# Optimization experiments

Hardware: AMD Instinct MI355X
Metric: run time of the kernel (lower is better)

The kernel has to match this reference:

```python
import jax, jax.numpy as jnp
import numpy as np

N = 2_000_000
C0 = 0.28209479177387814
C1 = 0.4886025119029199


def setup_inputs() -> dict:
    key = jax.random.key(0)
    ks = jax.random.split(key, 6)
    return {
        "view_dirs": jax.random.normal(ks[0], (N, 3), dtype=jnp.float32),
        "xyz": jax.random.uniform(ks[1], (N, 3), dtype=jnp.float32) * 2.0 - 1.0,
        "scale_log": jax.random.uniform(ks[2], (N, 3), dtype=jnp.float32) - 3.0,
        "rot_quat": jax.random.uniform(ks[3], (N, 4), dtype=jnp.float32),
        "opacity_logit": jax.random.uniform(ks[4], (N, 1), dtype=jnp.float32),
        "sh_coeffs": jax.random.uniform(ks[5], (N, 3, 4), dtype=jnp.float32),
    }


def _build_rotation(q):
    # F.normalize along dim=1 with eps=1e-12
    q = q / jnp.maximum(jnp.linalg.norm(q, axis=1, keepdims=True), 1e-12)
    r, x, y, z = q[:, 0], q[:, 1], q[:, 2], q[:, 3]
    R = jnp.stack([
        1 - 2 * (y * y + z * z), 2 * (x * y - r * z), 2 * (x * z + r * y),
        2 * (x * y + r * z), 1 - 2 * (x * x + z * z), 2 * (y * z - r * x),
        2 * (x * z - r * y), 2 * (y * z + r * x), 1 - 2 * (x * x + y * y),
    ], axis=-1).reshape(-1, 3, 3)
    return R


def _eval_sh(sh_coeffs, dirs):
    # degree = 1 -> 4 coeffs
    x, y, z = dirs[:, 0:1], dirs[:, 1:2], dirs[:, 2:3]  # [N,1] broadcast over color
    return (C0 * sh_coeffs[:, :, 0]
            - C1 * y * sh_coeffs[:, :, 1]
            + C1 * z * sh_coeffs[:, :, 2]
            - C1 * x * sh_coeffs[:, :, 3])


def reference(view_dirs, xyz, scale_log, rot_quat, opacity_logit, sh_coeffs):
    opacity = jax.nn.sigmoid(opacity_logit)                  # [N,1]
    scale = jnp.exp(scale_log)                               # [N,3]
    rgb = jax.nn.sigmoid(_eval_sh(sh_coeffs, view_dirs))     # [N,3]
    R = _build_rotation(rot_quat)                            # [N,3,3]
    M = R * scale[:, None, :]                                # R @ diag(scale), columns scaled
    cov3d = jnp.einsum('nij,nkj->nik', M, M)                 # M @ M^T
    return xyz, cov3d, rgb, opacity
```

## Files before the change

### kernel.cpp

```cpp
#include <hip/hip_runtime.h>

#define C0 0.28209479177387814f
#define C1 0.4886025119029199f

__device__ __forceinline__ float sigmoidf(float x) {
    return 1.0f / (1.0f + expf(-x));
}

__global__ __launch_bounds__(256) void gauss_kernel(
    const float* __restrict__ view_dirs,
    const float* __restrict__ xyz,
    const float* __restrict__ scale_log,
    const float4* __restrict__ rot_quat,
    const float* __restrict__ opacity_logit,
    const float4* __restrict__ sh,
    float* __restrict__ out_xyz,
    float* __restrict__ out_cov,
    float* __restrict__ out_rgb,
    float* __restrict__ out_op,
    int N)
{
    int i = blockIdx.x * blockDim.x + threadIdx.x;
    if (i >= N) return;

    float vx = view_dirs[3*i+0], vy = view_dirs[3*i+1], vz = view_dirs[3*i+2];
    float px = xyz[3*i+0],       py = xyz[3*i+1],       pz = xyz[3*i+2];
    float sl0 = scale_log[3*i+0], sl1 = scale_log[3*i+1], sl2 = scale_log[3*i+2];
    float4 q  = rot_quat[i];
    float  ol = opacity_logit[i];
    float4 c0 = sh[3*i+0];
    float4 c1 = sh[3*i+1];
    float4 c2 = sh[3*i+2];

    float opacity = sigmoidf(ol);

    float r0 = C0*c0.x - C1*vy*c0.y + C1*vz*c0.z - C1*vx*c0.w;
    float r1 = C0*c1.x - C1*vy*c1.y + C1*vz*c1.z - C1*vx*c1.w;
    float r2 = C0*c2.x - C1*vy*c2.y + C1*vz*c2.z - C1*vx*c2.w;
    r0 = sigmoidf(r0); r1 = sigmoidf(r1); r2 = sigmoidf(r2);

    float nrm = sqrtf(q.x*q.x + q.y*q.y + q.z*q.z + q.w*q.w);
    float inv = 1.0f / fmaxf(nrm, 1e-12f);
    float r = q.x*inv, x = q.y*inv, y = q.z*inv, z = q.w*inv;

    float R00 = 1.0f - 2.0f*(y*y + z*z);
    float R01 = 2.0f*(x*y - r*z);
    float R02 = 2.0f*(x*z + r*y);
    float R10 = 2.0f*(x*y + r*z);
    float R11 = 1.0f - 2.0f*(x*x + z*z);
    float R12 = 2.0f*(y*z - r*x);
    float R20 = 2.0f*(x*z - r*y);
    float R21 = 2.0f*(y*z + r*x);
    float R22 = 1.0f - 2.0f*(x*x + y*y);

    float s0 = expf(sl0), s1 = expf(sl1), s2 = expf(sl2);

    float M00 = R00*s0, M01 = R01*s1, M02 = R02*s2;
    float M10 = R10*s0, M11 = R11*s1, M12 = R12*s2;
    float M20 = R20*s0, M21 = R21*s1, M22 = R22*s2;

    float cv00 = M00*M00 + M01*M01 + M02*M02;
    float cv01 = M00*M10 + M01*M11 + M02*M12;
    float cv02 = M00*M20 + M01*M21 + M02*M22;
    float cv11 = M10*M10 + M11*M11 + M12*M12;
    float cv12 = M10*M20 + M11*M21 + M12*M22;
    float cv22 = M20*M20 + M21*M21 + M22*M22;

    out_xyz[3*i+0] = px; out_xyz[3*i+1] = py; out_xyz[3*i+2] = pz;

    float* cp = out_cov + 9*i;
    cp[0] = cv00; cp[1] = cv01; cp[2] = cv02;
    cp[3] = cv01; cp[4] = cv11; cp[5] = cv12;
    cp[6] = cv02; cp[7] = cv12; cp[8] = cv22;

    out_rgb[3*i+0] = r0; out_rgb[3*i+1] = r1; out_rgb[3*i+2] = r2;
    out_op[i] = opacity;
}

extern "C" void kernel_launch(void* const* d_in, const int* in_sizes, int n_in,
                              void* d_out, int out_size, void* d_ws, size_t ws_size,
                              hipStream_t stream) {
    const float*  view_dirs     = (const float*)d_in[0];
    const float*  xyz           = (const float*)d_in[1];
    const float*  scale_log     = (const float*)d_in[2];
    const float4* rot_quat      = (const float4*)d_in[3];
    const float*  opacity_logit = (const float*)d_in[4];
    const float4* sh            = (const float4*)d_in[5];

    int N = in_sizes[4];

    float* out = (float*)d_out;
    float* out_xyz = out;
    float* out_cov = out + (size_t)3*N;
    float* out_rgb = out + (size_t)12*N;
    float* out_op  = out + (size_t)15*N;

    int block = 256;
    int grid = (N + block - 1) / block;
    gauss_kernel<<<grid, block, 0, stream>>>(view_dirs, xyz, scale_log, rot_quat,
                                             opacity_logit, sh,
                                             out_xyz, out_cov, out_rgb, out_op, N);
}
```

Before: 279.2 us.

## Stage strided AoS loads and stores through LDS for coalesced global access

Each block cooperatively loads view_dirs, scale_log and SH coefficients into shared memory with unit-stride coalesced reads, padding the SH layout to avoid bank conflicts. Results are staged back in LDS, and xyz, rgb and covariance are written with coalesced unit-stride stores. The aim is to remove the stride-3, stride-9 and stride-12 uncoalesced accesses in this memory-bound kernel. In exchange it adds three block barriers and about 20KB of LDS per block, which may lower occupancy.

```diff
diff --git a/kernel.cpp b/kernel.cpp
--- a/kernel.cpp
+++ b/kernel.cpp
@@ -2,79 +2,130 @@
 
 #define C0 0.28209479177387814f
 #define C1 0.4886025119029199f
+#define BLK 256
 
 __device__ __forceinline__ float sigmoidf(float x) {
     return 1.0f / (1.0f + expf(-x));
 }
 
-__global__ __launch_bounds__(256) void gauss_kernel(
+__global__ __launch_bounds__(BLK) void gauss_kernel_lds(
     const float* __restrict__ view_dirs,
     const float* __restrict__ xyz,
     const float* __restrict__ scale_log,
     const float4* __restrict__ rot_quat,
     const float* __restrict__ opacity_logit,
-    const float4* __restrict__ sh,
+    const float* __restrict__ sh,
     float* __restrict__ out_xyz,
     float* __restrict__ out_cov,
     float* __restrict__ out_rgb,
     float* __restrict__ out_op,
     int N)
 {
-    int i = blockIdx.x * blockDim.x + threadIdx.x;
-    if (i >= N) return;
+    __shared__ float lds_sh[BLK * 13];
+    __shared__ float lds_vd[BLK * 3];
+    __shared__ float lds_sl[BLK * 3];
 
-    float vx = view_dirs[3*i+0], vy = view_dirs[3*i+1], vz = view_dirs[3*i+2];
-    float px = xyz[3*i+0],       py = xyz[3*i+1],       pz = xyz[3*i+2];
-    float sl0 = scale_log[3*i+0], sl1 = scale_log[3*i+1], sl2 = scale_log[3*i+2];
-    float4 q  = rot_quat[i];
-    float  ol = opacity_logit[i];
-    float4 c0 = sh[3*i+0];
-    float4 c1 = sh[3*i+1];
-    float4 c2 = sh[3*i+2];
+    const int t    = threadIdx.x;
+    const int base = blockIdx.x * BLK;
+    const int nblk = min(BLK, N - base);
+    const long b3  = (long)base * 3;
+    const long b9  = (long)base * 9;
+    const long b12 = (long)base * 12;
 
-    float opacity = sigmoidf(ol);
+    #pragma unroll
+    for (int j = 0; j < 3; ++j) {
+        int f = t + BLK * j;
+        if (f < nblk * 3) {
+            lds_vd[f] = view_dirs[b3 + f];
+            lds_sl[f] = scale_log[b3 + f];
+        }
+    }
+    #pragma unroll
+    for (int j = 0; j < 12; ++j) {
+        int f = t + BLK * j;
+        if (f < nblk * 12) {
+            lds_sh[f + f / 12] = sh[b12 + f];
+        }
+    }
+    __syncthreads();
 
-    float r0 = C0*c0.x - C1*vy*c0.y + C1*vz*c0.z - C1*vx*c0.w;
-    float r1 = C0*c1.x - C1*vy*c1.y + C1*vz*c1.z - C1*vx*c1.w;
-    float r2 = C0*c2.x - C1*vy*c2.y + C1*vz*c2.z - C1*vx*c2.w;
-    r0 = sigmoidf(r0); r1 = sigmoidf(r1); r2 = sigmoidf(r2);
+    const bool active = (t < nblk);
+    float vx = 0.f, vy = 0.f, vz = 0.f;
+    float sl0 = 0.f, sl1 = 0.f, sl2 = 0.f;
+    float c[12];
+    float4 q = make_float4(1.f, 0.f, 0.f, 0.f);
+    float ol = 0.f;
+    #pragma unroll
+    for (int m = 0; m < 12; ++m) c[m] = 0.f;
 
-    float nrm = sqrtf(q.x*q.x + q.y*q.y + q.z*q.z + q.w*q.w);
-    float inv = 1.0f / fmaxf(nrm, 1e-12f);
-    float r = q.x*inv, x = q.y*inv, y = q.z*inv, z = q.w*inv;
+    if (active) {
+        vx = lds_vd[3 * t + 0]; vy = lds_vd[3 * t + 1]; vz = lds_vd[3 * t + 2];
+        sl0 = lds_sl[3 * t + 0]; sl1 = lds_sl[3 * t + 1]; sl2 = lds_sl[3 * t + 2];
+        #pragma unroll
+        for (int m = 0; m < 12; ++m) c[m] = lds_sh[13 * t + m];
+        q  = rot_quat[base + t];
+        ol = opacity_logit[base + t];
+    }
+    __syncthreads();
 
-    float R00 = 1.0f - 2.0f*(y*y + z*z);
-    float R01 = 2.0f*(x*y - r*z);
-    float R02 = 2.0f*(x*z + r*y);
-    float R10 = 2.0f*(x*y + r*z);
-    float R11 = 1.0f - 2.0f*(x*x + z*z);
-    float R12 = 2.0f*(y*z - r*x);
-    float R20 = 2.0f*(x*z - r*y);
-    float R21 = 2.0f*(y*z + r*x);
-    float R22 = 1.0f - 2.0f*(x*x + y*y);
+    if (active) {
+        float r0 = C0 * c[0] - C1 * vy * c[1] + C1 * vz * c[2]  - C1 * vx * c[3];
+        float r1 = C0 * c[4] - C1 * vy * c[5] + C1 * vz * c[6]  - C1 * vx * c[7];
+        float r2 = C0 * c[8] - C1 * vy * c[9] + C1 * vz * c[10] - C1 * vx * c[11];
+        r0 = sigmoidf(r0); r1 = sigmoidf(r1); r2 = sigmoidf(r2);
 
-    float s0 = expf(sl0), s1 = expf(sl1), s2 = expf(sl2);
+        float nrm = sqrtf(q.x * q.x + q.y * q.y + q.z * q.z + q.w * q.w);
+        float inv = 1.0f / fmaxf(nrm, 1e-12f);
+        float r = q.x * inv, x = q.y * inv, y = q.z * inv, z = q.w * inv;
 
-    float M00 = R00*s0, M01 = R01*s1, M02 = R02*s2;
-    float M10 = R10*s0, M11 = R11*s1, M12 = R12*s2;
-    float M20 = R20*s0, M21 = R21*s1, M22 = R22*s2;
+        float R00 = 1.0f - 2.0f * (y * y + z * z);
+        float R01 = 2.0f * (x * y - r * z);
+        float R02 = 2.0f * (x * z + r * y);
+        float R10 = 2.0f * (x * y + r * z);
+        float R11 = 1.0f - 2.0f * (x * x + z * z);
+        float R12 = 2.0f * (y * z - r * x);
+        float R20 = 2.0f * (x * z - r * y);
+        float R21 = 2.0f * (y * z + r * x);
+        float R22 = 1.0f - 2.0f * (x * x + y * y);
 
-    float cv00 = M00*M00 + M01*M01 + M02*M02;
-    float cv01 = M00*M10 + M01*M11 + M02*M12;
-    float cv02 = M00*M20 + M01*M21 + M02*M22;
-    float cv11 = M10*M10 + M11*M11 + M12*M12;
-    float cv12 = M10*M20 + M11*M21 + M12*M22;
-    float cv22 = M20*M20 + M21*M21 + M22*M22;
+        float s0 = expf(sl0), s1 = expf(sl1), s2 = expf(sl2);
+        float M00 = R00 * s0, M01 = R01 * s1, M02 = R02 * s2;
+        float M10 = R10 * s0, M11 = R11 * s1, M12 = R12 * s2;
+        float M20 = R20 * s0, M21 = R21 * s1, M22 = R22 * s2;
 
-    out_xyz[3*i+0] = px; out_xyz[3*i+1] = py; out_xyz[3*i+2] = pz;
+        float cv00 = M00 * M00 + M01 * M01 + M02 * M02;
+        float cv01 = M00 * M10 + M01 * M11 + M02 * M12;
+        float cv02 = M00 * M20 + M01 * M21 + M02 * M22;
+        float cv11 = M10 * M10 + M11 * M11 + M12 * M12;
+        float cv12 = M10 * M20 + M11 * M21 + M12 * M22;
+        float cv22 = M20 * M20 + M21 * M21 + M22 * M22;
 
-    float* cp = out_cov + 9*i;
-    cp[0] = cv00; cp[1] = cv01; cp[2] = cv02;
-    cp[3] = cv01; cp[4] = cv11; cp[5] = cv12;
-    cp[6] = cv02; cp[7] = cv12; cp[8] = cv22;
+        float* cov = lds_sh;
+        cov[9 * t + 0] = cv00; cov[9 * t + 1] = cv01; cov[9 * t + 2] = cv02;
+        cov[9 * t + 3] = cv01; cov[9 * t + 4] = cv11; cov[9 * t + 5] = cv12;
+        cov[9 * t + 6] = cv02; cov[9 * t + 7] = cv12; cov[9 * t + 8] = cv22;
 
-    out_rgb[3*i+0] = r0; out_rgb[3*i+1] = r1; out_rgb[3*i+2] = r2;
-    out_op[i] = opacity;
+        lds_vd[3 * t + 0] = r0; lds_vd[3 * t + 1] = r1; lds_vd[3 * t + 2] = r2;
+
+        out_op[base + t] = sigmoidf(ol);
+    }
+    __syncthreads();
+
+    #pragma unroll
+    for (int j = 0; j < 3; ++j) {
+        int f = t + BLK * j;
+        if (f < nblk * 3) {
+            out_xyz[b3 + f] = xyz[b3 + f];
+            out_rgb[b3 + f] = lds_vd[f];
+        }
+    }
+    #pragma unroll
+    for (int j = 0; j < 9; ++j) {
+        int f = t + BLK * j;
+        if (f < nblk * 9) {
+            out_cov[b9 + f] = lds_sh[f];
+        }
+    }
 }
 
 extern "C" void kernel_launch(void* const* d_in, const int* in_sizes, int n_in,
@@ -85,7 +136,7 @@
     const float*  scale_log     = (const float*)d_in[2];
     const float4* rot_quat      = (const float4*)d_in[3];
     const float*  opacity_logit = (const float*)d_in[4];
-    const float4* sh            = (const float4*)d_in[5];
+    const float*  sh            = (const float*)d_in[5];
 
     int N = in_sizes[4];
 
@@ -95,9 +146,8 @@
     float* out_rgb = out + (size_t)12*N;
     float* out_op  = out + (size_t)15*N;
 
-    int block = 256;
-    int grid = (N + block - 1) / block;
-    gauss_kernel<<<grid, block, 0, stream>>>(view_dirs, xyz, scale_log, rot_quat,
-                                             opacity_logit, sh,
-                                             out_xyz, out_cov, out_rgb, out_op, N);
+    int grid = (N + BLK - 1) / BLK;
+    gauss_kernel_lds<<<grid, BLK, 0, stream>>>(view_dirs, xyz, scale_log, rot_quat,
+                                               opacity_logit, sh,
+                                               out_xyz, out_cov, out_rgb, out_op, N);
 }
```

After: 286.5 us. 1.03x slower.

## Stage stride-3 and stride-9 accesses through LDS with vectorized coalesced loads/stores

Applied to the files above, without the earlier changes.

Adds a kernel that loads view_dirs, scale_log and SH coefficients as coalesced 16-byte vectors into shared memory, using a padded layout for the SH block. Each thread computes from LDS, then the cov, rgb and xyz outputs are staged back through LDS and written as float4 nontemporal stores. The aim is to replace strided scalar global accesses with fully coalesced wide transactions in this bandwidth-bound kernel. The cost is extra LDS traffic, three barriers and possible bank conflicts. The scalar kernel is kept as a fallback when N is not a multiple of 4.

```diff
diff --git a/kernel.cpp b/kernel.cpp
--- a/kernel.cpp
+++ b/kernel.cpp
@@ -2,12 +2,177 @@
 
 #define C0 0.28209479177387814f
 #define C1 0.4886025119029199f
+#define BLK 256
+
+typedef float f4 __attribute__((ext_vector_type(4)));
 
 __device__ __forceinline__ float sigmoidf(float x) {
     return 1.0f / (1.0f + expf(-x));
 }
 
-__global__ __launch_bounds__(256) void gauss_kernel(
+__global__ __launch_bounds__(BLK) void gauss_kernel_lds4(
+    const float* __restrict__ view_dirs,
+    const float* __restrict__ xyz,
+    const float* __restrict__ scale_log,
+    const float4* __restrict__ rot_quat,
+    const float* __restrict__ opacity_logit,
+    const float* __restrict__ sh,
+    float* __restrict__ out_xyz,
+    float* __restrict__ out_cov,
+    float* __restrict__ out_rgb,
+    float* __restrict__ out_op,
+    int N)
+{
+    __shared__ float lds_sh[BLK * 13];
+    __shared__ float lds_vd[BLK * 3];
+    __shared__ float lds_sl[BLK * 3];
+
+    const int t    = threadIdx.x;
+    const int base = blockIdx.x * BLK;
+    const int nblk = min(BLK, N - base);
+    const long b3  = (long)base * 3;
+    const long b9  = (long)base * 9;
+    const long b12 = (long)base * 12;
+    const bool full = (nblk == BLK);
+
+    if (full) {
+        const f4* vd4 = (const f4*)(view_dirs + b3);
+        const f4* sl4 = (const f4*)(scale_log + b3);
+        const f4* sh4 = (const f4*)(sh + b12);
+        if (t < 192) {
+            f4 v = vd4[t];
+            lds_vd[4*t+0] = v.x; lds_vd[4*t+1] = v.y;
+            lds_vd[4*t+2] = v.z; lds_vd[4*t+3] = v.w;
+            f4 s = sl4[t];
+            lds_sl[4*t+0] = s.x; lds_sl[4*t+1] = s.y;
+            lds_sl[4*t+2] = s.z; lds_sl[4*t+3] = s.w;
+        }
+        #pragma unroll
+        for (int j = 0; j < 3; ++j) {
+            int f4i = t + BLK * j;
+            f4 v = sh4[f4i];
+            int e = f4i / 3, c4 = f4i % 3;
+            int a = 13 * e + 4 * c4;
+            lds_sh[a+0] = v.x; lds_sh[a+1] = v.y;
+            lds_sh[a+2] = v.z; lds_sh[a+3] = v.w;
+        }
+    } else {
+        #pragma unroll
+        for (int j = 0; j < 3; ++j) {
+            int f = t + BLK * j;
+            if (f < nblk * 3) {
+                lds_vd[f] = view_dirs[b3 + f];
+                lds_sl[f] = scale_log[b3 + f];
+            }
+        }
+        #pragma unroll
+        for (int j = 0; j < 12; ++j) {
+            int f = t + BLK * j;
+            if (f < nblk * 12) lds_sh[f + f / 12] = sh[b12 + f];
+        }
+    }
+    __syncthreads();
+
+    const bool active = (t < nblk);
+    float vx = 0.f, vy = 0.f, vz = 0.f;
+    float sl0 = 0.f, sl1 = 0.f, sl2 = 0.f;
+    float c[12];
+    float4 q = make_float4(1.f, 0.f, 0.f, 0.f);
+    float ol = 0.f;
+    #pragma unroll
+    for (int m = 0; m < 12; ++m) c[m] = 0.f;
+
+    if (active) {
+        vx = lds_vd[3*t+0]; vy = lds_vd[3*t+1]; vz = lds_vd[3*t+2];
+        sl0 = lds_sl[3*t+0]; sl1 = lds_sl[3*t+1]; sl2 = lds_sl[3*t+2];
+        #pragma unroll
+        for (int m = 0; m < 12; ++m) c[m] = lds_sh[13*t + m];
+        q  = rot_quat[base + t];
+        ol = opacity_logit[base + t];
+    }
+    __syncthreads();
+
+    if (active) {
+        float r0 = C0*c[0] - C1*vy*c[1] + C1*vz*c[2]  - C1*vx*c[3];
+        float r1 = C0*c[4] - C1*vy*c[5] + C1*vz*c[6]  - C1*vx*c[7];
+        float r2 = C0*c[8] - C1*vy*c[9] + C1*vz*c[10] - C1*vx*c[11];
+        r0 = sigmoidf(r0); r1 = sigmoidf(r1); r2 = sigmoidf(r2);
+
+        float nrm = sqrtf(q.x*q.x + q.y*q.y + q.z*q.z + q.w*q.w);
+        float inv = 1.0f / fmaxf(nrm, 1e-12f);
+        float r = q.x*inv, x = q.y*inv, y = q.z*inv, z = q.w*inv;
+
+        float R00 = 1.0f - 2.0f*(y*y + z*z);
+        float R01 = 2.0f*(x*y - r*z);
+        float R02 = 2.0f*(x*z + r*y);
+        float R10 = 2.0f*(x*y + r*z);
+        float R11 = 1.0f - 2.0f*(x*x + z*z);
+        float R12 = 2.0f*(y*z - r*x);
+        float R20 = 2.0f*(x*z - r*y);
+        float R21 = 2.0f*(y*z + r*x);
+        float R22 = 1.0f - 2.0f*(x*x + y*y);
+
+        float s0 = expf(sl0), s1 = expf(sl1), s2 = expf(sl2);
+        float M00 = R00*s0, M01 = R01*s1, M02 = R02*s2;
+        float M10 = R10*s0, M11 = R11*s1, M12 = R12*s2;
+        float M20 = R20*s0, M21 = R21*s1, M22 = R22*s2;
+
+        float cv00 = M00*M00 + M01*M01 + M02*M02;
+        float cv01 = M00*M10 + M01*M11 + M02*M12;
+        float cv02 = M00*M20 + M01*M21 + M02*M22;
+        float cv11 = M10*M10 + M11*M11 + M12*M12;
+        float cv12 = M10*M20 + M11*M21 + M12*M22;
+        float cv22 = M20*M20 + M21*M21 + M22*M22;
+
+        float* cov = lds_sh;
+        cov[9*t+0] = cv00; cov[9*t+1] = cv01; cov[9*t+2] = cv02;
+        cov[9*t+3] = cv01; cov[9*t+4] = cv11; cov[9*t+5] = cv12;
+        cov[9*t+6] = cv02; cov[9*t+7] = cv12; cov[9*t+8] = cv22;
+
+        lds_vd[3*t+0] = r0; lds_vd[3*t+1] = r1; lds_vd[3*t+2] = r2;
+
+        __builtin_nontemporal_store(sigmoidf(ol), out_op + base + t);
+    }
+    __syncthreads();
+
+    if (full) {
+        const f4* xi4 = (const f4*)(xyz     + b3);
+        f4* ox4 = (f4*)(out_xyz + b3);
+        f4* or4 = (f4*)(out_rgb + b3);
+        f4* oc4 = (f4*)(out_cov + b9);
+        if (t < 192) {
+            f4 p = xi4[t];
+            __builtin_nontemporal_store(p, ox4 + t);
+            f4 rg = *(const f4*)(lds_vd + 4*t);
+            __builtin_nontemporal_store(rg, or4 + t);
+        }
+        #pragma unroll
+        for (int j = 0; j < 3; ++j) {
+            int f4i = t + BLK * j;
+            if (f4i < 576) {
+                f4 cv = *(const f4*)(lds_sh + 4*f4i);
+                __builtin_nontemporal_store(cv, oc4 + f4i);
+            }
+        }
+    } else {
+        #pragma unroll
+        for (int j = 0; j < 3; ++j) {
+            int f = t + BLK * j;
+            if (f < nblk * 3) {
+                __builtin_nontemporal_store(xyz[b3 + f], out_xyz + b3 + f);
+                __builtin_nontemporal_store(lds_vd[f],  out_rgb + b3 + f);
+            }
+        }
+        #pragma unroll
+        for (int j = 0; j < 9; ++j) {
+            int f = t + BLK * j;
+            if (f < nblk * 9)
+                __builtin_nontemporal_store(lds_sh[f], out_cov + b9 + f);
+        }
+    }
+}
+
+__global__ __launch_bounds__(BLK) void gauss_kernel_scalar(
     const float* __restrict__ view_dirs,
     const float* __restrict__ xyz,
     const float* __restrict__ scale_log,
@@ -24,37 +189,26 @@
     if (i >= N) return;
 
     float vx = view_dirs[3*i+0], vy = view_dirs[3*i+1], vz = view_dirs[3*i+2];
-    float px = xyz[3*i+0],       py = xyz[3*i+1],       pz = xyz[3*i+2];
+    float px = xyz[3*i+0], py = xyz[3*i+1], pz = xyz[3*i+2];
     float sl0 = scale_log[3*i+0], sl1 = scale_log[3*i+1], sl2 = scale_log[3*i+2];
-    float4 q  = rot_quat[i];
-    float  ol = opacity_logit[i];
-    float4 c0 = sh[3*i+0];
-    float4 c1 = sh[3*i+1];
-    float4 c2 = sh[3*i+2];
+    float4 q = rot_quat[i];
+    float ol = opacity_logit[i];
+    float4 c0 = sh[3*i+0], c1 = sh[3*i+1], c2 = sh[3*i+2];
 
     float opacity = sigmoidf(ol);
-
-    float r0 = C0*c0.x - C1*vy*c0.y + C1*vz*c0.z - C1*vx*c0.w;
-    float r1 = C0*c1.x - C1*vy*c1.y + C1*vz*c1.z - C1*vx*c1.w;
-    float r2 = C0*c2.x - C1*vy*c2.y + C1*vz*c2.z - C1*vx*c2.w;
-    r0 = sigmoidf(r0); r1 = sigmoidf(r1); r2 = sigmoidf(r2);
+    float r0 = sigmoidf(C0*c0.x - C1*vy*c0.y + C1*vz*c0.z - C1*vx*c0.w);
+    float r1 = sigmoidf(C0*c1.x - C1*vy*c1.y + C1*vz*c1.z - C1*vx*c1.w);
+    float r2 = sigmoidf(C0*c2.x - C1*vy*c2.y + C1*vz*c2.z - C1*vx*c2.w);
 
     float nrm = sqrtf(q.x*q.x + q.y*q.y + q.z*q.z + q.w*q.w);
     float inv = 1.0f / fmaxf(nrm, 1e-12f);
     float r = q.x*inv, x = q.y*inv, y = q.z*inv, z = q.w*inv;
 
-    float R00 = 1.0f - 2.0f*(y*y + z*z);
-    float R01 = 2.0f*(x*y - r*z);
-    float R02 = 2.0f*(x*z + r*y);
-    float R10 = 2.0f*(x*y + r*z);
-    float R11 = 1.0f - 2.0f*(x*x + z*z);
-    float R12 = 2.0f*(y*z - r*x);
-    float R20 = 2.0f*(x*z - r*y);
-    float R21 = 2.0f*(y*z + r*x);
-    float R22 = 1.0f - 2.0f*(x*x + y*y);
+    float R00 = 1.0f - 2.0f*(y*y + z*z), R01 = 2.0f*(x*y - r*z), R02 = 2.0f*(x*z + r*y);
+    float R10 = 2.0f*(x*y + r*z), R11 = 1.0f - 2.0f*(x*x + z*z), R12 = 2.0f*(y*z - r*x);
+    float R20 = 2.0f*(x*z - r*y), R21 = 2.0f*(y*z + r*x), R22 = 1.0f - 2.0f*(x*x + y*y);
 
     float s0 = expf(sl0), s1 = expf(sl1), s2 = expf(sl2);
-
     float M00 = R00*s0, M01 = R01*s1, M02 = R02*s2;
     float M10 = R10*s0, M11 = R11*s1, M12 = R12*s2;
     float M20 = R20*s0, M21 = R21*s1, M22 = R22*s2;
@@ -67,12 +221,10 @@
     float cv22 = M20*M20 + M21*M21 + M22*M22;
 
     out_xyz[3*i+0] = px; out_xyz[3*i+1] = py; out_xyz[3*i+2] = pz;
-
     float* cp = out_cov + 9*i;
     cp[0] = cv00; cp[1] = cv01; cp[2] = cv02;
     cp[3] = cv01; cp[4] = cv11; cp[5] = cv12;
     cp[6] = cv02; cp[7] = cv12; cp[8] = cv22;
-
     out_rgb[3*i+0] = r0; out_rgb[3*i+1] = r1; out_rgb[3*i+2] = r2;
     out_op[i] = opacity;
 }
@@ -85,7 +237,7 @@
     const float*  scale_log     = (const float*)d_in[2];
     const float4* rot_quat      = (const float4*)d_in[3];
     const float*  opacity_logit = (const float*)d_in[4];
-    const float4* sh            = (const float4*)d_in[5];
+    const float*  sh            = (const float*)d_in[5];
 
     int N = in_sizes[4];
 
@@ -95,9 +247,17 @@
     float* out_rgb = out + (size_t)12*N;
     float* out_op  = out + (size_t)15*N;
 
-    int block = 256;
-    int grid = (N + block - 1) / block;
-    gauss_kernel<<<grid, block, 0, stream>>>(view_dirs, xyz, scale_log, rot_quat,
-                                             opacity_logit, sh,
-                                             out_xyz, out_cov, out_rgb, out_op, N);
-}
+    int grid = (N + BLK - 1) / BLK;
+    if ((N & 3) == 0) {
+        gauss_kernel_lds4<<<grid, BLK, 0, stream>>>(view_dirs, xyz, scale_log,
+                                                    rot_quat, opacity_logit, sh,
+                                                    out_xyz, out_cov, out_rgb,
+                                                    out_op, N);
+    } else {
+        gauss_kernel_scalar<<<grid, BLK, 0, stream>>>(view_dirs, xyz, scale_log,
+                                                      rot_quat, opacity_logit,
+                                                      (const float4*)sh,
+                                                      out_xyz, out_cov, out_rgb,
+                                                      out_op, N);
+    }
+}
```

Result: slower. 285.4 us (+2.2%).
